# Optimization experiments

Measured on AMD Instinct MI355X. Metric: run time of the kernel, lower is better.

Reference implementation:

```python
import jax, jax.numpy as jnp
import numpy as np

B, C, H, W = 8, 32, 512, 512
BN_EPS = 1e-5


def setup_inputs() -> dict:
    key = jax.random.key(0)
    k1, k2, k3, k4 = jax.random.split(key, 4)
    x = jax.random.normal(k1, (B, C, H, W), dtype=jnp.float32)
    # 1x1 conv weight: [out=4, in=4*C] (kaiming-like scale)
    w_compress = jax.random.normal(k2, (4, 4 * C), dtype=jnp.float32) / np.sqrt(4 * C)
    gamma = jnp.ones((4,), dtype=jnp.float32)
    beta = jnp.zeros((4,), dtype=jnp.float32)
    return {"x": x, "w_compress": w_compress, "gamma": gamma, "beta": beta}


def _four_dir(x):
    # zero-pad H and W by 1; shifted view at (di, dj) gives x[i+di, j+dj]
    xp = jnp.pad(x, ((0, 0), (0, 0), (1, 1), (1, 1)))

    def sh(di, dj):
        return jax.lax.dynamic_slice(xp, (0, 0, 1 + di, 1 + dj), x.shape)

    # PyTorch conv = cross-correlation: kernel one at (r,c) reads x[i+r-1, j+c-1]
    ne = sh(-1, +1) - x
    nw = sh(-1, -1) - x
    se = sh(+1, +1) - x
    sw = sh(+1, -1) - x
    return jnp.concatenate([ne, nw, se, sw], axis=1)  # [B, 4C, H, W]


def reference(x, w_compress, gamma, beta):
    feat = _four_dir(x)
    # 1x1 conv: channel mixing 4C -> 4
    y = jnp.einsum("oc,bchw->bohw", w_compress, feat)
    # BatchNorm2d (training mode: batch statistics, biased variance)
    mean = jnp.mean(y, axis=(0, 2, 3), keepdims=True)
    var = jnp.var(y, axis=(0, 2, 3), keepdims=True)
    y_hat = (y - mean) * jax.lax.rsqrt(var + BN_EPS)
    return y_hat * gamma[None, :, None, None] + beta[None, :, None, None]
```

## Files before the change

### kernel.cpp

```cpp
#include <hip/hip_runtime.h>

#define B_ 8
#define C_ 32
#define H_ 512
#define W_ 512
#define HW_ (H_ * W_)
#define BN_EPS 1e-5f


__global__ __launch_bounds__(256) void fourdir_compute(
    const float* __restrict__ x,
    const float* __restrict__ w,
    float* __restrict__ y,
    float* __restrict__ sums)
{
    __shared__ float4 wl4[5][C_];
    const int t = threadIdx.x;
    {
        float* wl = (float*)wl4;
        for (int idx = t; idx < 4 * 4 * C_; idx += 256) {
            int o  = idx & 3;
            int dc = idx >> 2;
            wl[idx] = w[o * (4 * C_) + dc];
        }
    }
    __syncthreads();
    if (t < 4 * C_) {
        float* wl = (float*)wl4;
        wl[512 + t] = -(wl[t] + wl[128 + t] + wl[256 + t] + wl[384 + t]);
    }
    __syncthreads();

    const int j     = (blockIdx.x << 6) + (t & 63);
    const int strip = t >> 6;
    const int i0    = (blockIdx.y << 4) + (strip << 2);
    const int b     = blockIdx.z;

    const float* xb = x + (size_t)b * C_ * HW_;
    const bool jm = (j > 0), jp = (j < W_ - 1);

    float4 acc[4];
#pragma unroll
    for (int p = 0; p < 4; ++p) acc[p] = make_float4(0.f, 0.f, 0.f, 0.f);

    for (int c = 0; c < C_; ++c) {
        const float* xc = xb + (size_t)c * HW_;
        float xl[6], xr[6], xm[4];
#pragma unroll
        for (int k = 0; k < 6; ++k) {
            const int r = i0 - 1 + k;
            const bool rv = (r >= 0) && (r < H_);
            const long off = (long)r * W_ + j;
            xl[k] = (rv && jm) ? xc[off - 1] : 0.f;
            xr[k] = (rv && jp) ? xc[off + 1] : 0.f;
        }
#pragma unroll
        for (int k = 0; k < 4; ++k) xm[k] = xc[(size_t)(i0 + k) * W_ + j];

        const float4 wne = wl4[0][c];
        const float4 wnw = wl4[1][c];
        const float4 wse = wl4[2][c];
        const float4 wsw = wl4[3][c];
        const float4 wct = wl4[4][c];
#pragma unroll
        for (int p = 0; p < 4; ++p) {
            acc[p].x += wne.x * xr[p] + wnw.x * xl[p] + wse.x * xr[p + 2] + wsw.x * xl[p + 2] + wct.x * xm[p];
            acc[p].y += wne.y * xr[p] + wnw.y * xl[p] + wse.y * xr[p + 2] + wsw.y * xl[p + 2] + wct.y * xm[p];
            acc[p].z += wne.z * xr[p] + wnw.z * xl[p] + wse.z * xr[p + 2] + wsw.z * xl[p + 2] + wct.z * xm[p];
            acc[p].w += wne.w * xr[p] + wnw.w * xl[p] + wse.w * xr[p + 2] + wsw.w * xl[p + 2] + wct.w * xm[p];
        }
    }

#pragma unroll
    for (int p = 0; p < 4; ++p) {
        const size_t row = (size_t)(i0 + p) * W_ + j;
        y[((size_t)b * 4 + 0) * HW_ + row] = acc[p].x;
        y[((size_t)b * 4 + 1) * HW_ + row] = acc[p].y;
        y[((size_t)b * 4 + 2) * HW_ + row] = acc[p].z;
        y[((size_t)b * 4 + 3) * HW_ + row] = acc[p].w;
    }

    float vals[8];
    vals[0] = acc[0].x + acc[1].x + acc[2].x + acc[3].x;
    vals[1] = acc[0].y + acc[1].y + acc[2].y + acc[3].y;
    vals[2] = acc[0].z + acc[1].z + acc[2].z + acc[3].z;
    vals[3] = acc[0].w + acc[1].w + acc[2].w + acc[3].w;
    vals[4] = acc[0].x * acc[0].x + acc[1].x * acc[1].x + acc[2].x * acc[2].x + acc[3].x * acc[3].x;
    vals[5] = acc[0].y * acc[0].y + acc[1].y * acc[1].y + acc[2].y * acc[2].y + acc[3].y * acc[3].y;
    vals[6] = acc[0].z * acc[0].z + acc[1].z * acc[1].z + acc[2].z * acc[2].z + acc[3].z * acc[3].z;
    vals[7] = acc[0].w * acc[0].w + acc[1].w * acc[1].w + acc[2].w * acc[2].w + acc[3].w * acc[3].w;

#pragma unroll
    for (int k = 0; k < 8; ++k) {
        float v = vals[k];
#pragma unroll
        for (int off = 32; off >= 1; off >>= 1) v += __shfl_xor(v, off, 64);
        vals[k] = v;
    }

    __shared__ float red[4][8];
    const int wave = t >> 6;
    const int lane = t & 63;
    if (lane == 0) {
#pragma unroll
        for (int k = 0; k < 8; ++k) red[wave][k] = vals[k];
    }
    __syncthreads();
    if (t < 8) {
        const float s = red[0][t] + red[1][t] + red[2][t] + red[3][t];
        atomicAdd(&sums[t], s);
    }
}

__global__ __launch_bounds__(256) void bn_norm(
    float* __restrict__ y,
    const float* __restrict__ sums,
    const float* __restrict__ gamma,
    const float* __restrict__ beta)
{
    const int gid = blockIdx.x * 256 + threadIdx.x;
    const size_t base = (size_t)gid * 4;
    const int o = (int)((base / HW_) & 3);

    const float n = (float)((size_t)B_ * HW_);
    const float mean  = sums[o] / n;
    const float var   = sums[4 + o] / n - mean * mean;
    const float scale = rsqrtf(var + BN_EPS) * gamma[o];
    const float shift = beta[o] - mean * scale;

    float4 v = *(const float4*)(y + base);
    v.x = v.x * scale + shift;
    v.y = v.y * scale + shift;
    v.z = v.z * scale + shift;
    v.w = v.w * scale + shift;
    *(float4*)(y + base) = v;
}

extern "C" void kernel_launch(void* const* d_in, const int* in_sizes, int n_in,
                              void* d_out, int out_size, void* d_ws, size_t ws_size,
                              hipStream_t stream) {
    const float* x     = (const float*)d_in[0];
    const float* w     = (const float*)d_in[1];
    const float* gamma = (const float*)d_in[2];
    const float* beta  = (const float*)d_in[3];
    float* out  = (float*)d_out;
    float* sums = (float*)d_ws;

    hipMemsetAsync(sums, 0, 8 * sizeof(float), stream);

    dim3 gridA(W_ / 64, H_ / 16, B_);
    fourdir_compute<<<gridA, 256, 0, stream>>>(x, w, out, sums);

    const int nf4 = (B_ * 4 * HW_) / 4;
    bn_norm<<<nf4 / 256, 256, 0, stream>>>(out, sums, gamma, beta);
}
```

Before: 414.7 us.

## Register-block two columns per thread with float4 row loads and edge-specialized path

Each thread now computes a 4x2 output tile instead of a 4x1 column strip. It loads six 4-wide row segments per channel with vectorized (possibly unaligned) 16-byte loads, replacing sixteen scalar loads for four outputs. A template splits border blocks, which shift and zero lanes, from interior blocks that skip the masking. Block height doubles, so the grid halves in y, and outputs are stored as float2. The aim is to cut load-instruction count and redundant neighbor reads. The cost is misaligned vector loads, more accumulator registers and fewer blocks in flight.

```diff
diff --git a/kernel.cpp b/kernel.cpp
--- a/kernel.cpp
+++ b/kernel.cpp
@@ -7,6 +7,74 @@
 #define HW_ (H_ * W_)
 #define BN_EPS 1e-5f
 
+
+typedef float f4v __attribute__((ext_vector_type(4)));
+
+template <bool EDGE>
+__device__ __forceinline__ void conv_body(
+    const float* __restrict__ xb, const float4 (*__restrict__ wl4)[C_],
+    int i0, int j0, float acc[4][2][4])
+{
+    int jb = j0 - 1;
+    bool le = false, re = false;
+    if (EDGE) {
+        le = (j0 == 0);
+        re = (j0 == W_ - 2);
+        if (le) jb = 0;
+        if (re) jb = W_ - 4;
+    }
+    const bool rv0 = (i0 > 0);
+    const bool rv5 = (i0 + 4 < H_);
+    const int rows[6] = {rv0 ? i0 - 1 : 0, i0, i0 + 1, i0 + 2, i0 + 3,
+                         rv5 ? i0 + 4 : H_ - 1};
+    int off[6];
+#pragma unroll
+    for (int k = 0; k < 6; ++k) off[k] = rows[k] * W_ + jb;
+
+    for (int c = 0; c < C_; ++c) {
+        const float* xc = xb + (size_t)c * HW_;
+        float v[6][4];
+#pragma unroll
+        for (int k = 0; k < 6; ++k) {
+            f4v ld;
+            __builtin_memcpy(&ld, xc + off[k], 16);
+            float a0 = ld.x, a1 = ld.y, a2 = ld.z, a3 = ld.w;
+            if (EDGE) {
+                if (le) { a0 = 0.f; a1 = ld.x; a2 = ld.y; a3 = ld.z; }
+                if (re) { a0 = ld.y; a1 = ld.z; a2 = ld.w; a3 = 0.f; }
+            }
+            v[k][0] = a0; v[k][1] = a1; v[k][2] = a2; v[k][3] = a3;
+        }
+        if (!rv0) { v[0][0] = v[0][1] = v[0][2] = v[0][3] = 0.f; }
+        if (!rv5) { v[5][0] = v[5][1] = v[5][2] = v[5][3] = 0.f; }
+
+        const float4 wne = wl4[0][c];
+        const float4 wnw = wl4[1][c];
+        const float4 wse = wl4[2][c];
+        const float4 wsw = wl4[3][c];
+        const float4 wct = wl4[4][c];
+        const float wneA[4] = {wne.x, wne.y, wne.z, wne.w};
+        const float wnwA[4] = {wnw.x, wnw.y, wnw.z, wnw.w};
+        const float wseA[4] = {wse.x, wse.y, wse.z, wse.w};
+        const float wswA[4] = {wsw.x, wsw.y, wsw.z, wsw.w};
+        const float wctA[4] = {wct.x, wct.y, wct.z, wct.w};
+
+#pragma unroll
+        for (int p = 0; p < 4; ++p)
+#pragma unroll
+            for (int q = 0; q < 2; ++q) {
+                const float ne = v[p][q + 2];
+                const float nw = v[p][q];
+                const float se = v[p + 2][q + 2];
+                const float sw = v[p + 2][q];
+                const float ct = v[p + 1][q + 1];
+#pragma unroll
+                for (int o = 0; o < 4; ++o)
+                    acc[p][q][o] += wneA[o] * ne + wnwA[o] * nw +
+                                    wseA[o] * se + wswA[o] * sw + wctA[o] * ct;
+            }
+    }
+}
 
 __global__ __launch_bounds__(256) void fourdir_compute(
     const float* __restrict__ x,
@@ -31,64 +99,49 @@
     }
     __syncthreads();
 
-    const int j     = (blockIdx.x << 6) + (t & 63);
-    const int strip = t >> 6;
-    const int i0    = (blockIdx.y << 4) + (strip << 2);
-    const int b     = blockIdx.z;
-
+    const int cg    = t & 31;
+    const int strip = t >> 5;
+    const int j0 = (blockIdx.x << 6) + (cg << 1);
+    const int i0 = (blockIdx.y << 5) + (strip << 2);
+    const int b  = blockIdx.z;
     const float* xb = x + (size_t)b * C_ * HW_;
-    const bool jm = (j > 0), jp = (j < W_ - 1);
-
-    float4 acc[4];
-#pragma unroll
-    for (int p = 0; p < 4; ++p) acc[p] = make_float4(0.f, 0.f, 0.f, 0.f);
-
-    for (int c = 0; c < C_; ++c) {
-        const float* xc = xb + (size_t)c * HW_;
-        float xl[6], xr[6], xm[4];
-#pragma unroll
-        for (int k = 0; k < 6; ++k) {
-            const int r = i0 - 1 + k;
-            const bool rv = (r >= 0) && (r < H_);
-            const long off = (long)r * W_ + j;
-            xl[k] = (rv && jm) ? xc[off - 1] : 0.f;
-            xr[k] = (rv && jp) ? xc[off + 1] : 0.f;
+
+    float acc[4][2][4];
+#pragma unroll
+    for (int p = 0; p < 4; ++p)
+#pragma unroll
+        for (int q = 0; q < 2; ++q)
+#pragma unroll
+            for (int o = 0; o < 4; ++o) acc[p][q][o] = 0.f;
+
+    if (blockIdx.x == 0 || blockIdx.x == (W_ / 64) - 1)
+        conv_body<true>(xb, wl4, i0, j0, acc);
+    else
+        conv_body<false>(xb, wl4, i0, j0, acc);
+
+#pragma unroll
+    for (int p = 0; p < 4; ++p) {
+        const size_t base = (size_t)(i0 + p) * W_ + j0;
+#pragma unroll
+        for (int o = 0; o < 4; ++o) {
+            *(float2*)(y + ((size_t)(b * 4 + o)) * HW_ + base) =
+                make_float2(acc[p][0][o], acc[p][1][o]);
         }
-#pragma unroll
-        for (int k = 0; k < 4; ++k) xm[k] = xc[(size_t)(i0 + k) * W_ + j];
-
-        const float4 wne = wl4[0][c];
-        const float4 wnw = wl4[1][c];
-        const float4 wse = wl4[2][c];
-        const float4 wsw = wl4[3][c];
-        const float4 wct = wl4[4][c];
-#pragma unroll
-        for (int p = 0; p < 4; ++p) {
-            acc[p].x += wne.x * xr[p] + wnw.x * xl[p] + wse.x * xr[p + 2] + wsw.x * xl[p + 2] + wct.x * xm[p];
-            acc[p].y += wne.y * xr[p] + wnw.y * xl[p] + wse.y * xr[p + 2] + wsw.y * xl[p + 2] + wct.y * xm[p];
-            acc[p].z += wne.z * xr[p] + wnw.z * xl[p] + wse.z * xr[p + 2] + wsw.z * xl[p + 2] + wct.z * xm[p];
-            acc[p].w += wne.w * xr[p] + wnw.w * xl[p] + wse.w * xr[p + 2] + wsw.w * xl[p + 2] + wct.w * xm[p];
-        }
-    }
-
-#pragma unroll
-    for (int p = 0; p < 4; ++p) {
-        const size_t row = (size_t)(i0 + p) * W_ + j;
-        y[((size_t)b * 4 + 0) * HW_ + row] = acc[p].x;
-        y[((size_t)b * 4 + 1) * HW_ + row] = acc[p].y;
-        y[((size_t)b * 4 + 2) * HW_ + row] = acc[p].z;
-        y[((size_t)b * 4 + 3) * HW_ + row] = acc[p].w;
     }
 
     float vals[8];
-    vals[0] = acc[0].x + acc[1].x + acc[2].x + acc[3].x;
-    vals[1] = acc[0].y + acc[1].y + acc[2].y + acc[3].y;
-    vals[2] = acc[0].z + acc[1].z + acc[2].z + acc[3].z;
-    vals[3] = acc[0].w + acc[1].w + acc[2].w + acc[3].w;
-    vals[4] = acc[0].x * acc[0].x + acc[1].x * acc[1].x + acc[2].x * acc[2].x + acc[3].x * acc[3].x;
-    vals[5] = acc[0].y * acc[0].y + acc[1].y * acc[1].y + acc[2].y * acc[2].y + acc[3].y * acc[3].y;
-    vals[6] = acc[0].z * acc[0].z + acc[1].z * acc[1].z + acc[2].z * acc[2].z + acc[3].z * acc[3].z;
-    vals[7] = acc[0].w * acc[0].w + acc[1].w * acc[1].w + acc[2].w * acc[2].w + acc[3].w * acc[3].w;
+#pragma unroll
+    for (int o = 0; o < 4; ++o) { vals[o] = 0.f; vals[4 + o] = 0.f; }
+#pragma unroll
+    for (int p = 0; p < 4; ++p)
+#pragma unroll
+        for (int q = 0; q < 2; ++q)
+#pragma unroll
+            for (int o = 0; o < 4; ++o) {
+                const float a = acc[p][q][o];
+                vals[o]     += a;
+                vals[4 + o] += a * a;
+            }
 
 #pragma unroll
     for (int k = 0; k < 8; ++k) {
@@ -148,7 +201,7 @@
 
     hipMemsetAsync(sums, 0, 8 * sizeof(float), stream);
 
-    dim3 gridA(W_ / 64, H_ / 16, B_);
+    dim3 gridA(W_ / 64, H_ / 32, B_);
     fourdir_compute<<<gridA, 256, 0, stream>>>(x, w, out, sums);
 
     const int nf4 = (B_ * 4 * HW_) / 4;
```

New measurement: 395.7 us. 1.05x faster.

## Compute 4x4 pixel tiles per thread with float4 row loads

Applied to the files above, without the earlier changes.

Each thread now produces a 4x4 output tile instead of a 4x1 column. It loads six float4 rows plus scalar left and right halo values per channel, which cuts redundant scalar neighbour loads and raises arithmetic per byte loaded. Outputs are written as float4 stores, and the grid shrinks to 64x64 tiles per block. The cost is many more accumulator registers (64 floats), capped by a launch bound of 2 blocks per SIMD, and fewer blocks in flight (512 total).

```diff
diff --git a/kernel.cpp b/kernel.cpp
--- a/kernel.cpp
+++ b/kernel.cpp
@@ -7,14 +7,16 @@
 #define HW_ (H_ * W_)
 #define BN_EPS 1e-5f
 
+typedef float f4v __attribute__((ext_vector_type(4)));
 
-__global__ __launch_bounds__(256) void fourdir_compute(
+
+__global__ __launch_bounds__(256, 2) void fourdir_compute(
     const float* __restrict__ x,
     const float* __restrict__ w,
     float* __restrict__ y,
     float* __restrict__ sums)
 {
-    __shared__ float4 wl4[5][C_];
+    __shared__ f4v wl4[5][C_];
     const int t = threadIdx.x;
     {
         float* wl = (float*)wl4;
@@ -31,79 +33,100 @@
     }
     __syncthreads();
 
-    const int j     = (blockIdx.x << 6) + (t & 63);
-    const int strip = t >> 6;
-    const int i0    = (blockIdx.y << 4) + (strip << 2);
-    const int b     = blockIdx.z;
+    const int lane = t & 63;
+    const int wv   = t >> 6;
+    const int cg   = lane & 15;
+    const int sr   = lane >> 4;
+    const int j0 = (blockIdx.x << 6) + (cg << 2);
+    const int i0 = (blockIdx.y << 6) + (wv << 4) + (sr << 2);
+    const int b  = blockIdx.z;
+    const float* xb = x + (size_t)b * C_ * HW_;
 
-    const float* xb = x + (size_t)b * C_ * HW_;
-    const bool jm = (j > 0), jp = (j < W_ - 1);
+    const bool jm = (j0 > 0);
+    const bool jp = (j0 + 4 < W_);
+    const bool tv = (i0 > 0);
+    const bool bv = (i0 + 4 < H_);
 
-    float4 acc[4];
+    int off[6];
+    {
+        const int rows[6] = { tv ? i0 - 1 : 0, i0, i0 + 1, i0 + 2, i0 + 3,
+                              bv ? i0 + 4 : H_ - 1 };
 #pragma unroll
-    for (int p = 0; p < 4; ++p) acc[p] = make_float4(0.f, 0.f, 0.f, 0.f);
+        for (int k = 0; k < 6; ++k) off[k] = rows[k] * W_ + j0;
+    }
 
+    f4v acc[4][4];
+#pragma unroll
+    for (int p = 0; p < 4; ++p)
+#pragma unroll
+        for (int q = 0; q < 4; ++q) acc[p][q] = f4v{0.f, 0.f, 0.f, 0.f};
+
+#pragma unroll 2
     for (int c = 0; c < C_; ++c) {
         const float* xc = xb + (size_t)c * HW_;
-        float xl[6], xr[6], xm[4];
+        f4v  vr[6];
+        float lf[6], rt[6];
 #pragma unroll
         for (int k = 0; k < 6; ++k) {
-            const int r = i0 - 1 + k;
-            const bool rv = (r >= 0) && (r < H_);
-            const long off = (long)r * W_ + j;
-            xl[k] = (rv && jm) ? xc[off - 1] : 0.f;
-            xr[k] = (rv && jp) ? xc[off + 1] : 0.f;
+            vr[k] = *(const f4v*)(xc + off[k]);
+            lf[k] = jm ? xc[off[k] - 1] : 0.f;
+            rt[k] = jp ? xc[off[k] + 4] : 0.f;
         }
-#pragma unroll
-        for (int k = 0; k < 4; ++k) xm[k] = xc[(size_t)(i0 + k) * W_ + j];
+        if (!tv) { vr[0] = f4v{0.f,0.f,0.f,0.f}; lf[0] = 0.f; rt[0] = 0.f; }
+        if (!bv) { vr[5] = f4v{0.f,0.f,0.f,0.f}; lf[5] = 0.f; rt[5] = 0.f; }
 
-        const float4 wne = wl4[0][c];
-        const float4 wnw = wl4[1][c];
-        const float4 wse = wl4[2][c];
-        const float4 wsw = wl4[3][c];
-        const float4 wct = wl4[4][c];
+        const f4v wne = wl4[0][c];
+        const f4v wnw = wl4[1][c];
+        const f4v wse = wl4[2][c];
+        const f4v wsw = wl4[3][c];
+        const f4v wct = wl4[4][c];
+
 #pragma unroll
         for (int p = 0; p < 4; ++p) {
-            acc[p].x += wne.x * xr[p] + wnw.x * xl[p] + wse.x * xr[p + 2] + wsw.x * xl[p + 2] + wct.x * xm[p];
-            acc[p].y += wne.y * xr[p] + wnw.y * xl[p] + wse.y * xr[p + 2] + wsw.y * xl[p + 2] + wct.y * xm[p];
-            acc[p].z += wne.z * xr[p] + wnw.z * xl[p] + wse.z * xr[p + 2] + wsw.z * xl[p + 2] + wct.z * xm[p];
-            acc[p].w += wne.w * xr[p] + wnw.w * xl[p] + wse.w * xr[p + 2] + wsw.w * xl[p + 2] + wct.w * xm[p];
+#pragma unroll
+            for (int q = 0; q < 4; ++q) {
+                const float ne = (q < 3) ? vr[p][q + 1]     : rt[p];
+                const float nw = (q > 0) ? vr[p][q - 1]     : lf[p];
+                const float se = (q < 3) ? vr[p + 2][q + 1] : rt[p + 2];
+                const float sw = (q > 0) ? vr[p + 2][q - 1] : lf[p + 2];
+                const float ct = vr[p + 1][q];
+                acc[p][q] += wne * ne + wnw * nw + wse * se + wsw * sw + wct * ct;
+            }
         }
     }
 
 #pragma unroll
     for (int p = 0; p < 4; ++p) {
-        const size_t row = (size_t)(i0 + p) * W_ + j;
-        y[((size_t)b * 4 + 0) * HW_ + row] = acc[p].x;
-        y[((size_t)b * 4 + 1) * HW_ + row] = acc[p].y;
-        y[((size_t)b * 4 + 2) * HW_ + row] = acc[p].z;
-        y[((size_t)b * 4 + 3) * HW_ + row] = acc[p].w;
+        const size_t base = (size_t)(i0 + p) * W_ + j0;
+#pragma unroll
+        for (int o = 0; o < 4; ++o) {
+            f4v st = { acc[p][0][o], acc[p][1][o], acc[p][2][o], acc[p][3][o] };
+            *(f4v*)(y + ((size_t)(b * 4 + o)) * HW_ + base) = st;
+        }
     }
 
-    float vals[8];
-    vals[0] = acc[0].x + acc[1].x + acc[2].x + acc[3].x;
-    vals[1] = acc[0].y + acc[1].y + acc[2].y + acc[3].y;
-    vals[2] = acc[0].z + acc[1].z + acc[2].z + acc[3].z;
-    vals[3] = acc[0].w + acc[1].w + acc[2].w + acc[3].w;
-    vals[4] = acc[0].x * acc[0].x + acc[1].x * acc[1].x + acc[2].x * acc[2].x + acc[3].x * acc[3].x;
-    vals[5] = acc[0].y * acc[0].y + acc[1].y * acc[1].y + acc[2].y * acc[2].y + acc[3].y * acc[3].y;
-    vals[6] = acc[0].z * acc[0].z + acc[1].z * acc[1].z + acc[2].z * acc[2].z + acc[3].z * acc[3].z;
-    vals[7] = acc[0].w * acc[0].w + acc[1].w * acc[1].w + acc[2].w * acc[2].w + acc[3].w * acc[3].w;
+    f4v s0 = f4v{0.f,0.f,0.f,0.f}, s1 = f4v{0.f,0.f,0.f,0.f};
+#pragma unroll
+    for (int p = 0; p < 4; ++p)
+#pragma unroll
+        for (int q = 0; q < 4; ++q) {
+            s0 += acc[p][q];
+            s1 += acc[p][q] * acc[p][q];
+        }
 
+    float vals[8] = { s0[0], s0[1], s0[2], s0[3], s1[0], s1[1], s1[2], s1[3] };
 #pragma unroll
     for (int k = 0; k < 8; ++k) {
         float v = vals[k];
 #pragma unroll
-        for (int off = 32; off >= 1; off >>= 1) v += __shfl_xor(v, off, 64);
+        for (int o = 32; o >= 1; o >>= 1) v += __shfl_xor(v, o, 64);
         vals[k] = v;
     }
 
     __shared__ float red[4][8];
-    const int wave = t >> 6;
-    const int lane = t & 63;
     if (lane == 0) {
 #pragma unroll
-        for (int k = 0; k < 8; ++k) red[wave][k] = vals[k];
+        for (int k = 0; k < 8; ++k) red[wv][k] = vals[k];
     }
     __syncthreads();
     if (t < 8) {
@@ -148,7 +171,7 @@
 
     hipMemsetAsync(sums, 0, 8 * sizeof(float), stream);
 
-    dim3 gridA(W_ / 64, H_ / 16, B_);
+    dim3 gridA(W_ / 64, H_ / 64, B_);
     fourdir_compute<<<gridA, 256, 0, stream>>>(x, w, out, sums);
 
     const int nf4 = (B_ * 4 * HW_) / 4;
```

New measurement: 394.4 us. 4.9% less time.
